# Kernel optimization log

Hardware: AMD Instinct MI355X
Metric: run time of the kernel (lower is better)

The kernel has to match this reference:

```python
import jax, jax.numpy as jnp
import numpy as np

N, E, G = 20000, 320000, 256
CAT, CONT, NEL = 16, 8, 9
HC, HE, HID, H, OUT = 32, 32, 64, 4, 128


def _gatv2(h, src, tgt, ee, Wl, bl, Wr, br, We, att, bias):
    # PyG GATv2Conv (eval mode, flow=source_to_target): messages aggregated at tgt
    n = h.shape[0]
    Hh, C = att.shape
    xl = (h @ Wl + bl).reshape(n, Hh, C)   # source transform
    xr = (h @ Wr + br).reshape(n, Hh, C)   # target transform
    ep = (ee @ We).reshape(-1, Hh, C)      # edge transform (no bias in PyG)
    m = jax.nn.leaky_relu(xl[src] + xr[tgt] + ep, 0.2)  # [E,H,C]
    e = jnp.einsum('ehc,hc->eh', m, att)                # [E,H]
    emax = jax.ops.segment_max(e, tgt, num_segments=n)
    p = jnp.exp(e - emax[tgt])
    denom = jax.ops.segment_sum(p, tgt, num_segments=n)
    alpha = p / (denom[tgt] + 1e-16)
    out = jax.ops.segment_sum(alpha[..., None] * xl[src], tgt, num_segments=n)
    return out.reshape(n, Hh * C) + bias


def setup_inputs() -> dict:
    key = jax.random.key(0)
    k = jax.random.split(key, 26)
    f = jnp.float32
    def w(kk, i, o):
        return jax.random.normal(kk, (i, o), f) / np.float32(np.sqrt(i))
    return {
        'x': jax.random.normal(k[0], (N, CAT + CONT), f),
        'edge_index': jax.random.randint(k[1], (2, E), 0, N, jnp.int32),
        'edge_attr': jax.random.uniform(k[2], (E, NEL), f),
        'batch': jnp.sort(jax.random.randint(k[3], (N,), 0, G, jnp.int32)),
        'W_cat': w(k[4], CAT, HC), 'b_cat': jnp.zeros((HC,), f),
        'W_e': w(k[5], NEL, HE), 'b_e': jnp.zeros((HE,), f),
        'W_init': w(k[6], CONT + HC, HID), 'b_init': jnp.zeros((HID,), f),
        'Wl1': w(k[7], HID, H * HID), 'bl1': jnp.zeros((H * HID,), f),
        'Wr1': w(k[8], HID, H * HID), 'br1': jnp.zeros((H * HID,), f),
        'We1': w(k[9], HE, H * HID),
        'att1': jax.random.normal(k[10], (H, HID), f) / np.float32(np.sqrt(HID)),
        'bias1': jnp.zeros((H * HID,), f),
        'Wl2': w(k[11], H * HID, HID), 'bl2': jnp.zeros((HID,), f),
        'Wr2': w(k[12], H * HID, HID), 'br2': jnp.zeros((HID,), f),
        'We2': w(k[13], HE, HID),
        'att2': jax.random.normal(k[14], (1, HID), f) / np.float32(np.sqrt(HID)),
        'bias2': jnp.zeros((HID,), f),
        'W_out': w(k[15], HID, OUT), 'b_out': jnp.zeros((OUT,), f),
    }


def reference(x, edge_index, edge_attr, batch,
              W_cat, b_cat, W_e, b_e, W_init, b_init,
              Wl1, bl1, Wr1, br1, We1, att1, bias1,
              Wl2, bl2, Wr2, br2, We2, att2, bias2,
              W_out, b_out):
    n = x.shape[0]
    f = x.dtype
    s = jax.nn.relu(x[:, :CAT] @ W_cat + b_cat)
    h = jnp.concatenate([x[:, CAT:], s], axis=1)
    h = jax.nn.relu(h @ W_init + b_init)
    ee = edge_attr @ W_e + b_e                       # [E, HE]
    src, tgt = edge_index[0], edge_index[1]
    # PyG GATv2Conv add_self_loops=True, fill_value='mean' on edge features
    cnt = jax.ops.segment_sum(jnp.ones((src.shape[0],), f), tgt, num_segments=n)
    loop_attr = jax.ops.segment_sum(ee, tgt, num_segments=n) / jnp.maximum(cnt, 1.0)[:, None]
    ar = jnp.arange(n, dtype=src.dtype)
    src2 = jnp.concatenate([src, ar])
    tgt2 = jnp.concatenate([tgt, ar])
    ee2 = jnp.concatenate([ee, loop_attr], axis=0)
    h = jax.nn.elu(_gatv2(h, src2, tgt2, ee2, Wl1, bl1, Wr1, br1, We1, att1, bias1))
    h = jax.nn.elu(_gatv2(h, src2, tgt2, ee2, Wl2, bl2, Wr2, br2, We2, att2, bias2))
    # global_mean_pool over graphs
    gcnt = jax.ops.segment_sum(jnp.ones((n,), f), batch, num_segments=G)
    pooled = jax.ops.segment_sum(h, batch, num_segments=G) / jnp.maximum(gcnt, 1.0)[:, None]
    return pooled @ W_out + b_out
```

## Files before the change

kernel.cpp:

```cpp
#include <hip/hip_runtime.h>
#include <hip/hip_bf16.h>

#define NN 20000
#define EE 320000
#define GG 256

__device__ __forceinline__ float lanebc(float v, int l){
  return __uint_as_float(__builtin_amdgcn_readlane(__float_as_uint(v), (unsigned)l));
}
__device__ __forceinline__ int lanebci(int v, int l){
  return __builtin_amdgcn_readlane(v, (unsigned)l);
}
__device__ __forceinline__ float wave_sum(float v){
  #pragma unroll
  for(int m=32;m>0;m>>=1) v += __shfl_xor(v, m, 64);
  return v;
}
__device__ __forceinline__ float wave_max(float v){
  #pragma unroll
  for(int m=32;m>0;m>>=1) v = fmaxf(v, __shfl_xor(v, m, 64));
  return v;
}
__device__ __forceinline__ float elu(float o){
  return (o > 0.f) ? o : (__expf(o) - 1.f);
}
__device__ __forceinline__ float bf2f(ushort u){ return __uint_as_float((unsigned)u << 16); }
__device__ __forceinline__ ushort f2bf(float f){
  unsigned x = __float_as_uint(f);
  return (ushort)((x + 0x7FFFu + ((x >> 16) & 1u)) >> 16);
}
__device__ __forceinline__ float2 up2(unsigned w){
  return make_float2(__uint_as_float(w << 16), __uint_as_float(w & 0xFFFF0000u));
}

template<int F>
__global__ void k_fold(const float* __restrict__ We9, const float* __restrict__ be,
                       const float* __restrict__ WeL, float* __restrict__ Wf, float* __restrict__ bf){
  const int c = threadIdx.x;
  #pragma unroll
  for (int j=0;j<9;j++){
    float a = 0.f;
    #pragma unroll
    for (int k=0;k<32;k++) a += We9[j*32+k]*WeL[k*F+c];
    Wf[j*F+c] = a;
  }
  float b = 0.f;
  #pragma unroll
  for (int k=0;k<32;k++) b += be[k]*WeL[k*F+c];
  bf[c] = b;
}

__global__ void k_prep(const float* __restrict__ Wl1, const float* __restrict__ Wl2,
                       const float* __restrict__ Wr2, float4* __restrict__ Wl1p4,
                       float4* __restrict__ Wl2p4, float4* __restrict__ Wr2p4){
  const int idx = (blockIdx.x%16)*256 + threadIdx.x;
  const int seg = blockIdx.x/16;
  if (seg == 0){
    const int k4 = idx>>8, c = idx&255;
    Wl1p4[idx] = make_float4(Wl1[(4*k4+0)*256+c], Wl1[(4*k4+1)*256+c],
                             Wl1[(4*k4+2)*256+c], Wl1[(4*k4+3)*256+c]);
  } else if (seg == 1){
    const int k4 = idx>>6, cc = idx&63;
    Wl2p4[idx] = make_float4(Wl2[(4*k4+0)*64+cc], Wl2[(4*k4+1)*64+cc],
                             Wl2[(4*k4+2)*64+cc], Wl2[(4*k4+3)*64+cc]);
  } else {
    const int k4 = idx>>6, cc = idx&63;
    Wr2p4[idx] = make_float4(Wr2[(4*k4+0)*64+cc], Wr2[(4*k4+1)*64+cc],
                             Wr2[(4*k4+2)*64+cc], Wr2[(4*k4+3)*64+cc]);
  }
}

__global__ void k_node_mlp(const float* __restrict__ x, const float* __restrict__ Wcat,
                           const float* __restrict__ bcat, const float* __restrict__ Wini,
                           const float* __restrict__ bini, float* __restrict__ h0,
                           ushort* __restrict__ h0b){
  const int t = blockIdx.x;
  const int c = threadIdx.x;
  __shared__ float xs[24];
  __shared__ float s[32];
  if (c < 24) xs[c] = x[t*24 + c];
  __syncthreads();
  if (c < 32){
    float a = bcat[c];
    #pragma unroll
    for(int k=0;k<16;k++) a += xs[k]*Wcat[k*32 + c];
    s[c] = fmaxf(a, 0.f);
  }
  __syncthreads();
  float a = bini[c];
  #pragma unroll
  for(int k=0;k<8;k++)  a += xs[16+k]*Wini[k*64 + c];
  #pragma unroll
  for(int k=0;k<32;k++) a += s[k]*Wini[(8+k)*64 + c];
  const float r = fmaxf(a, 0.f);
  h0[t*64 + c] = r;
  h0b[t*64 + c] = f2bf(r);
}

__global__ void k_edge_acc(const int* __restrict__ ei, const float* __restrict__ ea,
                           float* __restrict__ loopA, int* __restrict__ cnt){
  const int g = blockIdx.x*16 + (threadIdx.x>>4);
  const int j = threadIdx.x & 15;
  if (g >= EE) return;
  const int t = ei[EE + g];
  if (j < 9)       atomicAdd(&loopA[t*12 + j], ea[(size_t)g*9 + j]);
  else if (j == 9) atomicAdd(&cnt[t], 1);
}

__global__ void k_alloc(const int* __restrict__ cnt, int* __restrict__ start, int* __restrict__ counter){
  int i = blockIdx.x*blockDim.x + threadIdx.x;
  if (i < NN) start[i] = atomicAdd(counter, cnt[i]);
}

__global__ void k_scatter(const int* __restrict__ ei, const int* __restrict__ start,
                          int* __restrict__ fill, int* __restrict__ csr,
                          int* __restrict__ srcp, int* __restrict__ tgtp){
  int e = blockIdx.x*blockDim.x + threadIdx.x;
  if (e >= EE) return;
  int t = ei[EE + e];
  int p = start[t] + atomicAdd(&fill[t], 1);
  csr[p] = e;
  srcp[p] = ei[e];
  tgtp[p] = t;
}

__global__ void k_xlxr1(const float* __restrict__ h0, const float* __restrict__ Wl,
                        const float* __restrict__ bl, const float* __restrict__ Wr,
                        const float* __restrict__ br, ushort* __restrict__ xl, ushort* __restrict__ xr){
  const int n0 = blockIdx.x*8;
  __shared__ __align__(16) float hsT[64][8];
  for(int i=threadIdx.x;i<512;i+=256){ int n=i>>6, k=i&63; hsT[k][n] = h0[(n0+n)*64 + k]; }
  __syncthreads();
  const int c = threadIdx.x;
  float accl[8], accr[8];
  const float blv = bl[c], brv = br[c];
  #pragma unroll
  for(int n=0;n<8;n++){ accl[n]=blv; accr[n]=brv; }
  for(int k=0;k<64;k++){
    const float wl = Wl[k*256 + c];
    const float wr = Wr[k*256 + c];
    const float4 ha = *(const float4*)&hsT[k][0];
    const float4 hb = *(const float4*)&hsT[k][4];
    accl[0]+=ha.x*wl; accr[0]+=ha.x*wr; accl[1]+=ha.y*wl; accr[1]+=ha.y*wr;
    accl[2]+=ha.z*wl; accr[2]+=ha.z*wr; accl[3]+=ha.w*wl; accr[3]+=ha.w*wr;
    accl[4]+=hb.x*wl; accr[4]+=hb.x*wr; accl[5]+=hb.y*wl; accr[5]+=hb.y*wr;
    accl[6]+=hb.z*wl; accr[6]+=hb.z*wr; accl[7]+=hb.w*wl; accr[7]+=hb.w*wr;
  }
  #pragma unroll
  for(int n=0;n<8;n++){
    xl[(size_t)(n0+n)*256 + c] = f2bf(accl[n]);
    xr[(size_t)(n0+n)*256 + c] = f2bf(accr[n]);
  }
}

template<int F>
__global__ __launch_bounds__(256) void k_score(const float* __restrict__ ea, const int* __restrict__ csr,
                        const int* __restrict__ srcp, const int* __restrict__ tgtp,
                        const ushort* __restrict__ xl, const ushort* __restrict__ xr,
                        const float* __restrict__ Wf, const float* __restrict__ bf,
                        const float* __restrict__ att, float* __restrict__ esc)
{
  constexpr int HP  = (F == 256) ? 2 : 1;
  constexpr int CPL = (F == 256) ? 8 : 4;
  const int tid  = threadIdx.x;
  const int lane = tid & 63;
  const int w    = tid >> 6;
  const int p0   = blockIdx.x * 64;

  __shared__ float ea_sT[9][64];
  __shared__ float Wf_s[9*F];
  __shared__ float bf_s[F];
  __shared__ int csr_s[64], src_s[64], tgt_s[64];

  if (tid < 64) { csr_s[tid] = csr[p0+tid]; src_s[tid] = srcp[p0+tid]; tgt_s[tid] = tgtp[p0+tid]; }
  __syncthreads();
  for (int i = tid; i < 576; i += 256){ int j = i>>6, ed = i&63; ea_sT[j][ed] = ea[(size_t)csr_s[ed]*9 + j]; }
  for (int i = tid; i < (9*F)/4; i += 256) ((float4*)Wf_s)[i] = ((const float4*)Wf)[i];
  if (tid < F) bf_s[tid] = bf[tid];
  __syncthreads();

  const int g = lane >> 4, t = lane & 15;
  const int eb = w*16 + g*4;

  #pragma unroll
  for (int hp = 0; hp < HP; ++hp) {
    const int c = hp*(F/HP) + t*CPL;
    float bfv[CPL];
    *(float4*)&bfv[0] = *(const float4*)&bf_s[c];
    if (CPL==8) *(float4*)&bfv[4] = *(const float4*)&bf_s[c+4];
    float acc[4][CPL];
    #pragma unroll
    for (int j=0;j<4;j++)
      #pragma unroll
      for(int q=0;q<CPL;q++) acc[j][q]=bfv[q];
    #pragma unroll
    for (int k=0;k<9;k++){
      const float4 ev = *(const float4*)&ea_sT[k][eb];
      float wv[CPL];
      *(float4*)&wv[0] = *(const float4*)&Wf_s[k*F + c];
      if (CPL==8) *(float4*)&wv[4] = *(const float4*)&Wf_s[k*F + c + 4];
      #pragma unroll
      for (int q=0;q<CPL;q++){
        acc[0][q] += ev.x*wv[q]; acc[1][q] += ev.y*wv[q];
        acc[2][q] += ev.z*wv[q]; acc[3][q] += ev.w*wv[q];
      }
    }
    float attv[CPL];
    *(float4*)&attv[0] = *(const float4*)&att[c];
    if (CPL==8) *(float4*)&attv[4] = *(const float4*)&att[c+4];
    float partial[4];
    #pragma unroll
    for (int j=0;j<4;j++){
      const int s  = src_s[eb+j];
      const int tg = tgt_s[eb+j];
      float xlv[CPL], xrv[CPL];
      if (CPL==8){
        const uint4 a = *(const uint4*)&xl[(size_t)s*F + c];
        const uint4 b = *(const uint4*)&xr[(size_t)tg*F + c];
        float2 p;
        p=up2(a.x); xlv[0]=p.x; xlv[1]=p.y;  p=up2(a.y); xlv[2]=p.x; xlv[3]=p.y;
        p=up2(a.z); xlv[4]=p.x; xlv[5]=p.y;  p=up2(a.w); xlv[6]=p.x; xlv[7]=p.y;
        p=up2(b.x); xrv[0]=p.x; xrv[1]=p.y;  p=up2(b.y); xrv[2]=p.x; xrv[3]=p.y;
        p=up2(b.z); xrv[4]=p.x; xrv[5]=p.y;  p=up2(b.w); xrv[6]=p.x; xrv[7]=p.y;
      } else {
        const uint2 a = *(const uint2*)&xl[(size_t)s*F + c];
        const uint2 b = *(const uint2*)&xr[(size_t)tg*F + c];
        float2 p;
        p=up2(a.x); xlv[0]=p.x; xlv[1]=p.y;  p=up2(a.y); xlv[2]=p.x; xlv[3]=p.y;
        p=up2(b.x); xrv[0]=p.x; xrv[1]=p.y;  p=up2(b.y); xrv[2]=p.x; xrv[3]=p.y;
      }
      float sum = 0.f;
      #pragma unroll
      for (int q=0;q<CPL;q++){
        float m = acc[j][q] + xlv[q] + xrv[q];
        m = (m >= 0.f) ? m : 0.2f*m;
        sum += attv[q]*m;
      }
      partial[j] = sum;
    }
    #pragma unroll
    for (int j=0;j<4;j++){
      partial[j] += __shfl_xor(partial[j], 1, 64);
      partial[j] += __shfl_xor(partial[j], 2, 64);
      partial[j] += __shfl_xor(partial[j], 4, 64);
      if (F==64) partial[j] += __shfl_xor(partial[j], 8, 64);
    }
    if (F==256){
      if ((t & 7) == 0){
        const int h = hp*2 + (t>>3);
        #pragma unroll
        for (int j=0;j<4;j++) esc[(size_t)h*EE + p0 + eb + j] = partial[j];
      }
    } else {
      if (t == 0){
        #pragma unroll
        for (int j=0;j<4;j++) esc[p0 + eb + j] = partial[j];
      }
    }
  }
}

__global__ __launch_bounds__(256) void k_agg1(
    const float* __restrict__ loopA, const int* __restrict__ cnt,
    const int* __restrict__ start, const int* __restrict__ srcp,
    const ushort* __restrict__ h0b, const ushort* __restrict__ xl, const ushort* __restrict__ xr,
    const float* __restrict__ Wf, const float* __restrict__ bf,
    const float* __restrict__ att, const float* __restrict__ esc,
    float* __restrict__ zb)
{
  const int t = blockIdx.x*4 + (threadIdx.x>>6);
  const int c = threadIdx.x & 63;
  const int st = start[t], dg = cnt[t];

  float epb[4];
  if (dg > 0){
    const float invc = 1.f/(float)dg;
    float la[9];
    #pragma unroll
    for (int j=0;j<9;j++) la[j] = loopA[t*12+j]*invc;
    #pragma unroll
    for (int hd=0;hd<4;hd++){
      float ep = bf[hd*64+c];
      #pragma unroll
      for (int j=0;j<9;j++) ep += la[j]*Wf[j*256 + hd*64 + c];
      epb[hd] = ep;
    }
  } else {
    #pragma unroll
    for (int hd=0;hd<4;hd++) epb[hd]=0.f;
  }
  const float h0t = bf2f(h0b[(size_t)t*64 + c]);
  float sSelf[4];
  #pragma unroll
  for (int hd=0;hd<4;hd++){
    float m = bf2f(xl[(size_t)t*256 + hd*64 + c]) + bf2f(xr[(size_t)t*256 + hd*64 + c]) + epb[hd];
    m = (m>=0.f)? m : 0.2f*m;
    sSelf[hd] = wave_sum(att[hd*64+c]*m);
  }

  int sL = 0;
  float escv[4];
  #pragma unroll
  for (int hd=0;hd<4;hd++) escv[hd] = -1e30f;
  if (c < dg){
    sL = srcp[st+c];
    #pragma unroll
    for (int hd=0;hd<4;hd++) escv[hd] = esc[(size_t)hd*EE + st + c];
  }
  float mx[4];
  #pragma unroll
  for (int hd=0;hd<4;hd++) mx[hd] = fmaxf(wave_max(escv[hd]), sSelf[hd]);
  for (int i=64;i<dg;i+=64){
    #pragma unroll
    for (int hd=0;hd<4;hd++){
      float v = (i+c<dg)? esc[(size_t)hd*EE + st+i+c] : -1e30f;
      mx[hd] = fmaxf(mx[hd], wave_max(v));
    }
  }
  float preg[4], den[4], z[4];
  #pragma unroll
  for (int hd=0;hd<4;hd++){
    preg[hd] = (c<dg)? __expf(escv[hd]-mx[hd]) : 0.f;
    const float pS = __expf(sSelf[hd]-mx[hd]);
    den[hd] = wave_sum(preg[hd]) + pS;
    z[hd] = pS*h0t;
  }
  const int d1 = min(dg,64);
  for (int i=0;i<d1;i+=4){
    const int s0=lanebci(sL,i), s1=lanebci(sL,i+1), s2=lanebci(sL,i+2), s3=lanebci(sL,i+3);
    const float v0=bf2f(h0b[(size_t)s0*64+c]), v1=bf2f(h0b[(size_t)s1*64+c]);
    const float v2=bf2f(h0b[(size_t)s2*64+c]), v3=bf2f(h0b[(size_t)s3*64+c]);
    #pragma unroll
    for (int hd=0;hd<4;hd++){
      z[hd] += lanebc(preg[hd],i)*v0;
      z[hd] += lanebc(preg[hd],i+1)*v1;
      z[hd] += lanebc(preg[hd],i+2)*v2;
      z[hd] += lanebc(preg[hd],i+3)*v3;
    }
  }
  for (int i=64;i<dg;i++){
    const float hv = bf2f(h0b[(size_t)srcp[st+i]*64+c]);
    #pragma unroll
    for (int hd=0;hd<4;hd++){
      const float pp = __expf(esc[(size_t)hd*EE+st+i]-mx[hd]);
      den[hd] += pp;
      z[hd] += pp*hv;
    }
  }
  #pragma unroll
  for (int hd=0;hd<4;hd++) zb[(size_t)t*256 + hd*64 + c] = z[hd]/(den[hd]+1e-16f);
}

__global__ __launch_bounds__(256) void k_h1xlxr2(
    const float* __restrict__ zb, const float4* __restrict__ Wl1p4,
    const float* __restrict__ bl1, const float* __restrict__ bias1,
    const float4* __restrict__ Wl2p4, const float* __restrict__ bl2,
    const float4* __restrict__ Wr2p4, const float* __restrict__ br2,
    ushort* __restrict__ xl2, ushort* __restrict__ xr2)
{
  const int n0 = blockIdx.x*16;
  const int tid = threadIdx.x;
  __shared__ float zT[256*20];
  __shared__ __align__(16) float4 hs[64][17];
  #pragma unroll
  for (int j=0;j<16;j++) zT[tid*20 + j] = zb[(size_t)(n0+j)*256 + tid];
  __syncthreads();
  {
    const int c = tid, hd = c>>6;
    float acc[16];
    const float b = bl1[c] + bias1[c];
    #pragma unroll
    for (int n=0;n<16;n++) acc[n]=b;
    #pragma unroll 4
    for (int k4=0;k4<16;k4++){
      const float4 w4 = Wl1p4[k4*256 + c];
      #pragma unroll
      for (int kk=0;kk<4;kk++){
        const float wk = (kk==0)?w4.x:(kk==1)?w4.y:(kk==2)?w4.z:w4.w;
        const float* zr = &zT[(hd*64 + k4*4 + kk)*20];
        const float4 z0 = *(const float4*)&zr[0];
        const float4 z1 = *(const float4*)&zr[4];
        const float4 z2 = *(const float4*)&zr[8];
        const float4 z3 = *(const float4*)&zr[12];
        acc[0]+=z0.x*wk; acc[1]+=z0.y*wk; acc[2]+=z0.z*wk; acc[3]+=z0.w*wk;
        acc[4]+=z1.x*wk; acc[5]+=z1.y*wk; acc[6]+=z1.z*wk; acc[7]+=z1.w*wk;
        acc[8]+=z2.x*wk; acc[9]+=z2.y*wk; acc[10]+=z2.z*wk; acc[11]+=z2.w*wk;
        acc[12]+=z3.x*wk; acc[13]+=z3.y*wk; acc[14]+=z3.z*wk; acc[15]+=z3.w*wk;
      }
    }
    float* hsf = (float*)hs;
    const int base = (c>>2)*17*4 + (c&3);
    #pragma unroll
    for (int n=0;n<16;n++) hsf[base + n*4] = elu(acc[n]);
  }
  __syncthreads();
  {
    const int cc = tid & 63, ng = tid >> 6;
    float al[4], ar[4];
    const float bl = bl2[cc], br = br2[cc];
    #pragma unroll
    for (int j=0;j<4;j++){ al[j]=bl; ar[j]=br; }
    #pragma unroll 4
    for (int k4=0;k4<64;k4++){
      const float4 wl = Wl2p4[k4*64 + cc];
      const float4 wr = Wr2p4[k4*64 + cc];
      #pragma unroll
      for (int j=0;j<4;j++){
        const float4 hv = hs[k4][ng*4 + j];
        al[j] += hv.x*wl.x + hv.y*wl.y + hv.z*wl.z + hv.w*wl.w;
        ar[j] += hv.x*wr.x + hv.y*wr.y + hv.z*wr.z + hv.w*wr.w;
      }
    }
    #pragma unroll
    for (int j=0;j<4;j++){
      xl2[(size_t)(n0+ng*4+j)*64 + cc] = f2bf(al[j]);
      xr2[(size_t)(n0+ng*4+j)*64 + cc] = f2bf(ar[j]);
    }
  }
}

__global__ __launch_bounds__(256) void k_agg2(
    const float* __restrict__ loopA, const int* __restrict__ cnt,
    const int* __restrict__ start, const int* __restrict__ srcp,
    const ushort* __restrict__ xl, const ushort* __restrict__ xr,
    const float* __restrict__ Wf, const float* __restrict__ bf,
    const float* __restrict__ att, const float* __restrict__ bias,
    const float* __restrict__ esc, float* __restrict__ hout)
{
  const int t = blockIdx.x*4 + (threadIdx.x>>6);
  const int c = threadIdx.x & 63;
  const int st = start[t], dg = cnt[t];

  float ep = 0.f;
  if (dg>0){
    const float invc = 1.f/(float)dg;
    ep = bf[c];
    #pragma unroll
    for (int j=0;j<9;j++) ep += (loopA[t*12+j]*invc)*Wf[j*64+c];
  }
  const float xlt = bf2f(xl[(size_t)t*64+c]);
  float m = xlt + bf2f(xr[(size_t)t*64+c]) + ep;
  m = (m>=0.f)? m : 0.2f*m;
  const float sSelf = wave_sum(att[c]*m);

  int sL=0; float escv=-1e30f;
  if (c<dg){ sL=srcp[st+c]; escv=esc[st+c]; }
  float mx = fmaxf(wave_max(escv), sSelf);
  for (int i=64;i<dg;i+=64){
    float v=(i+c<dg)? esc[st+i+c] : -1e30f;
    mx = fmaxf(mx, wave_max(v));
  }
  float preg = (c<dg)? __expf(escv-mx) : 0.f;
  const float pS = __expf(sSelf-mx);
  float den = wave_sum(preg)+pS;
  float z = pS*xlt;
  const int d1=min(dg,64);
  for (int i=0;i<d1;i+=4){
    const int s0=lanebci(sL,i),s1=lanebci(sL,i+1),s2=lanebci(sL,i+2),s3=lanebci(sL,i+3);
    const float p0=lanebc(preg,i),p1=lanebc(preg,i+1),p2=lanebc(preg,i+2),p3=lanebc(preg,i+3);
    const float v0=bf2f(xl[(size_t)s0*64+c]),v1=bf2f(xl[(size_t)s1*64+c]);
    const float v2=bf2f(xl[(size_t)s2*64+c]),v3=bf2f(xl[(size_t)s3*64+c]);
    z += p0*v0; z += p1*v1; z += p2*v2; z += p3*v3;
  }
  for (int i=64;i<dg;i++){
    const float pp=__expf(esc[st+i]-mx); den+=pp;
    z += pp*bf2f(xl[(size_t)srcp[st+i]*64+c]);
  }
  const float o = z/(den+1e-16f)+bias[c];
  hout[(size_t)t*64+c] = elu(o);
}

__global__ void k_pool(const float* __restrict__ h2, const int* __restrict__ batch,
                       float* __restrict__ pooled, int* __restrict__ gcnt){
  int i = blockIdx.x*blockDim.x + threadIdx.x;
  if (i >= NN*64) return;
  int node = i >> 6, c = i & 63;
  int g = batch[node];
  atomicAdd(&pooled[g*64 + c], h2[i]);
  if (c == 0) atomicAdd(&gcnt[g], 1);
}

__global__ void k_out(const float* __restrict__ pooled, const int* __restrict__ gcnt,
                      const float* __restrict__ Wout, const float* __restrict__ bout,
                      float* __restrict__ out){
  int g = blockIdx.x, o = threadIdx.x;
  float a = 0.f;
  for(int k=0;k<64;k++) a += pooled[g*64 + k] * Wout[k*128 + o];
  float inv = 1.f / fmaxf((float)gcnt[g], 1.f);
  out[g*128 + o] = a*inv + bout[o];
}

extern "C" void kernel_launch(void* const* d_in, const int* in_sizes, int n_in,
                              void* d_out, int out_size, void* d_ws, size_t ws_size,
                              hipStream_t stream) {
  const float* x    = (const float*)d_in[0];
  const int*   ei   = (const int*)  d_in[1];
  const float* ea   = (const float*)d_in[2];
  const int*   batch= (const int*)  d_in[3];
  const float* Wcat = (const float*)d_in[4];
  const float* bcat = (const float*)d_in[5];
  const float* We   = (const float*)d_in[6];
  const float* be   = (const float*)d_in[7];
  const float* Wini = (const float*)d_in[8];
  const float* bini = (const float*)d_in[9];
  const float* Wl1  = (const float*)d_in[10];
  const float* bl1  = (const float*)d_in[11];
  const float* Wr1  = (const float*)d_in[12];
  const float* br1  = (const float*)d_in[13];
  const float* We1  = (const float*)d_in[14];
  const float* att1 = (const float*)d_in[15];
  const float* bias1= (const float*)d_in[16];
  const float* Wl2  = (const float*)d_in[17];
  const float* bl2  = (const float*)d_in[18];
  const float* Wr2  = (const float*)d_in[19];
  const float* br2  = (const float*)d_in[20];
  const float* We2  = (const float*)d_in[21];
  const float* att2 = (const float*)d_in[22];
  const float* bias2= (const float*)d_in[23];
  const float* Wout = (const float*)d_in[24];
  const float* bout = (const float*)d_in[25];
  float* out = (float*)d_out;
  char* ws = (char*)d_ws;

  size_t off = 0;
  auto alloc = [&](size_t bytes)->char*{ char* p = ws + off; off += (bytes + 255) & ~(size_t)255; return p; };
  float*  h0    = (float*) alloc((size_t)NN*64*4);
  ushort* h0b   = (ushort*)alloc((size_t)NN*64*2);
  float*  loopA = (float*) alloc((size_t)NN*12*4);
  ushort* xl1   = (ushort*)alloc((size_t)NN*256*2);
  ushort* xr1   = (ushort*)alloc((size_t)NN*256*2);
  float*  zb    = (float*) alloc((size_t)NN*256*4);
  ushort* xl2   = (ushort*)alloc((size_t)NN*64*2);
  ushort* xr2   = (ushort*)alloc((size_t)NN*64*2);
  float*  h2    = (float*) alloc((size_t)NN*64*4);
  float*  esc   = (float*) alloc((size_t)EE*4*4);
  float*  Wf1   = (float*) alloc((size_t)9*256*4);
  float*  bf1   = (float*) alloc((size_t)256*4);
  float*  Wf2   = (float*) alloc((size_t)9*64*4);
  float*  bf2   = (float*) alloc((size_t)64*4);
  float4* Wl1p4 = (float4*)alloc((size_t)4096*16);
  float4* Wl2p4 = (float4*)alloc((size_t)4096*16);
  float4* Wr2p4 = (float4*)alloc((size_t)4096*16);
  int*    cnt   = (int*)   alloc((size_t)NN*4);
  int*    start = (int*)   alloc((size_t)NN*4);
  int*    fill  = (int*)   alloc((size_t)NN*4);
  int*    csr   = (int*)   alloc((size_t)EE*4);
  int*    srcp  = (int*)   alloc((size_t)EE*4);
  int*    tgtp  = (int*)   alloc((size_t)EE*4);
  int*    counter = (int*) alloc(256);
  float*  pooled  = (float*)alloc((size_t)GG*64*4);
  int*    gcnt    = (int*)  alloc((size_t)GG*4);

  hipMemsetAsync(loopA,   0, (size_t)NN*12*4, stream);
  hipMemsetAsync(cnt,     0, (size_t)NN*4,    stream);
  hipMemsetAsync(fill,    0, (size_t)NN*4,    stream);
  hipMemsetAsync(counter, 0, 256,             stream);
  hipMemsetAsync(pooled,  0, (size_t)GG*64*4, stream);
  hipMemsetAsync(gcnt,    0, (size_t)GG*4,    stream);

  k_fold<256><<<1, 256, 0, stream>>>(We, be, We1, Wf1, bf1);
  k_fold<64> <<<1, 64, 0, stream>>>(We, be, We2, Wf2, bf2);
  k_prep     <<<48, 256, 0, stream>>>(Wl1, Wl2, Wr2, Wl1p4, Wl2p4, Wr2p4);
  k_node_mlp <<<NN, 64, 0, stream>>>(x, Wcat, bcat, Wini, bini, h0, h0b);
  k_edge_acc <<<EE/16, 256, 0, stream>>>(ei, ea, loopA, cnt);
  k_alloc    <<<(NN+255)/256, 256, 0, stream>>>(cnt, start, counter);
  k_scatter  <<<(EE+255)/256, 256, 0, stream>>>(ei, start, fill, csr, srcp, tgtp);
  k_xlxr1    <<<NN/8, 256, 0, stream>>>(h0, Wl1, bl1, Wr1, br1, xl1, xr1);
  k_score<256><<<EE/64, 256, 0, stream>>>(ea, csr, srcp, tgtp, xl1, xr1, Wf1, bf1, att1, esc);
  k_agg1     <<<NN/4, 256, 0, stream>>>(loopA, cnt, start, srcp, h0b, xl1, xr1, Wf1, bf1, att1, esc, zb);
  k_h1xlxr2  <<<NN/16, 256, 0, stream>>>(zb, Wl1p4, bl1, bias1, Wl2p4, bl2, Wr2p4, br2, xl2, xr2);
  k_score<64><<<EE/64, 256, 0, stream>>>(ea, csr, srcp, tgtp, xl2, xr2, Wf2, bf2, att2, esc);
  k_agg2     <<<NN/4, 256, 0, stream>>>(loopA, cnt, start, srcp, xl2, xr2, Wf2, bf2, att2, bias2, esc, h2);
  k_pool     <<<(NN*64+255)/256, 256, 0, stream>>>(h2, batch, pooled, gcnt);
  k_out      <<<GG, 128, 0, stream>>>(pooled, gcnt, Wout, bout, out);
}
```

Baseline: 339.5 us.

## Fuse node MLP, weight prep, pooling; drop softmax max pass; interleave scores

Merges the weight-folding and prep kernels into one launch and fuses the node MLP into the layer-1 xl/xr projection kernel. Global pooling is folded into the layer-2 aggregation, and the six memsets become one over a contiguous zeroed region. The softmax no longer computes a per-target max; it exponentiates raw scores clamped at 60, which removes a pass over the edge scores but risks overflow or precision loss for large scores. Layer-1 scores are stored interleaved by head so each edge's four heads load as one float4.

```diff
diff --git a/kernel.cpp b/kernel.cpp
--- a/kernel.cpp
+++ b/kernel.cpp
@@ -16,14 +16,10 @@
   for(int m=32;m>0;m>>=1) v += __shfl_xor(v, m, 64);
   return v;
 }
-__device__ __forceinline__ float wave_max(float v){
-  #pragma unroll
-  for(int m=32;m>0;m>>=1) v = fmaxf(v, __shfl_xor(v, m, 64));
-  return v;
-}
 __device__ __forceinline__ float elu(float o){
   return (o > 0.f) ? o : (__expf(o) - 1.f);
 }
+__device__ __forceinline__ float pexp(float e){ return __expf(fminf(e, 60.f)); }
 __device__ __forceinline__ float bf2f(ushort u){ return __uint_as_float((unsigned)u << 16); }
 __device__ __forceinline__ ushort f2bf(float f){
   unsigned x = __float_as_uint(f);
@@ -33,68 +29,61 @@
   return make_float2(__uint_as_float(w << 16), __uint_as_float(w & 0xFFFF0000u));
 }
 
-template<int F>
-__global__ void k_fold(const float* __restrict__ We9, const float* __restrict__ be,
-                       const float* __restrict__ WeL, float* __restrict__ Wf, float* __restrict__ bf){
-  const int c = threadIdx.x;
-  #pragma unroll
-  for (int j=0;j<9;j++){
-    float a = 0.f;
-    #pragma unroll
-    for (int k=0;k<32;k++) a += We9[j*32+k]*WeL[k*F+c];
-    Wf[j*F+c] = a;
-  }
-  float b = 0.f;
-  #pragma unroll
-  for (int k=0;k<32;k++) b += be[k]*WeL[k*F+c];
-  bf[c] = b;
-}
-
-__global__ void k_prep(const float* __restrict__ Wl1, const float* __restrict__ Wl2,
-                       const float* __restrict__ Wr2, float4* __restrict__ Wl1p4,
-                       float4* __restrict__ Wl2p4, float4* __restrict__ Wr2p4){
-  const int idx = (blockIdx.x%16)*256 + threadIdx.x;
-  const int seg = blockIdx.x/16;
-  if (seg == 0){
-    const int k4 = idx>>8, c = idx&255;
-    Wl1p4[idx] = make_float4(Wl1[(4*k4+0)*256+c], Wl1[(4*k4+1)*256+c],
-                             Wl1[(4*k4+2)*256+c], Wl1[(4*k4+3)*256+c]);
-  } else if (seg == 1){
-    const int k4 = idx>>6, cc = idx&63;
-    Wl2p4[idx] = make_float4(Wl2[(4*k4+0)*64+cc], Wl2[(4*k4+1)*64+cc],
-                             Wl2[(4*k4+2)*64+cc], Wl2[(4*k4+3)*64+cc]);
+__global__ void k_weights(const float* __restrict__ We9, const float* __restrict__ be,
+                          const float* __restrict__ We1, const float* __restrict__ We2,
+                          const float* __restrict__ Wl1, const float* __restrict__ Wl2,
+                          const float* __restrict__ Wr2,
+                          float* __restrict__ Wf1, float* __restrict__ bf1,
+                          float* __restrict__ Wf2, float* __restrict__ bf2,
+                          float4* __restrict__ Wl1p4, float4* __restrict__ Wl2p4,
+                          float4* __restrict__ Wr2p4){
+  const int b = blockIdx.x;
+  const int tid = threadIdx.x;
+  if (b < 48){
+    const int idx = (b%16)*256 + tid;
+    const int seg = b/16;
+    if (seg == 0){
+      const int k4 = idx>>8, c = idx&255;
+      Wl1p4[idx] = make_float4(Wl1[(4*k4+0)*256+c], Wl1[(4*k4+1)*256+c],
+                               Wl1[(4*k4+2)*256+c], Wl1[(4*k4+3)*256+c]);
+    } else if (seg == 1){
+      const int k4 = idx>>6, cc = idx&63;
+      Wl2p4[idx] = make_float4(Wl2[(4*k4+0)*64+cc], Wl2[(4*k4+1)*64+cc],
+                               Wl2[(4*k4+2)*64+cc], Wl2[(4*k4+3)*64+cc]);
+    } else {
+      const int k4 = idx>>6, cc = idx&63;
+      Wr2p4[idx] = make_float4(Wr2[(4*k4+0)*64+cc], Wr2[(4*k4+1)*64+cc],
+                               Wr2[(4*k4+2)*64+cc], Wr2[(4*k4+3)*64+cc]);
+    }
+  } else if (b == 48){
+    const int c = tid;
+    #pragma unroll
+    for (int j=0;j<9;j++){
+      float a = 0.f;
+      #pragma unroll
+      for (int k=0;k<32;k++) a += We9[j*32+k]*We1[k*256+c];
+      Wf1[j*256+c] = a;
+    }
+    float bb = 0.f;
+    #pragma unroll
+    for (int k=0;k<32;k++) bb += be[k]*We1[k*256+c];
+    bf1[c] = bb;
   } else {
-    const int k4 = idx>>6, cc = idx&63;
-    Wr2p4[idx] = make_float4(Wr2[(4*k4+0)*64+cc], Wr2[(4*k4+1)*64+cc],
-                             Wr2[(4*k4+2)*64+cc], Wr2[(4*k4+3)*64+cc]);
-  }
-}
-
-__global__ void k_node_mlp(const float* __restrict__ x, const float* __restrict__ Wcat,
-                           const float* __restrict__ bcat, const float* __restrict__ Wini,
-                           const float* __restrict__ bini, float* __restrict__ h0,
-                           ushort* __restrict__ h0b){
-  const int t = blockIdx.x;
-  const int c = threadIdx.x;
-  __shared__ float xs[24];
-  __shared__ float s[32];
-  if (c < 24) xs[c] = x[t*24 + c];
-  __syncthreads();
-  if (c < 32){
-    float a = bcat[c];
-    #pragma unroll
-    for(int k=0;k<16;k++) a += xs[k]*Wcat[k*32 + c];
-    s[c] = fmaxf(a, 0.f);
-  }
-  __syncthreads();
-  float a = bini[c];
-  #pragma unroll
-  for(int k=0;k<8;k++)  a += xs[16+k]*Wini[k*64 + c];
-  #pragma unroll
-  for(int k=0;k<32;k++) a += s[k]*Wini[(8+k)*64 + c];
-  const float r = fmaxf(a, 0.f);
-  h0[t*64 + c] = r;
-  h0b[t*64 + c] = f2bf(r);
+    if (tid < 64){
+      const int c = tid;
+      #pragma unroll
+      for (int j=0;j<9;j++){
+        float a = 0.f;
+        #pragma unroll
+        for (int k=0;k<32;k++) a += We9[j*32+k]*We2[k*64+c];
+        Wf2[j*64+c] = a;
+      }
+      float bb = 0.f;
+      #pragma unroll
+      for (int k=0;k<32;k++) bb += be[k]*We2[k*64+c];
+      bf2[c] = bb;
+    }
+  }
 }
 
 __global__ void k_edge_acc(const int* __restrict__ ei, const float* __restrict__ ea,
@@ -124,14 +113,43 @@
   tgtp[p] = t;
 }
 
-__global__ void k_xlxr1(const float* __restrict__ h0, const float* __restrict__ Wl,
-                        const float* __restrict__ bl, const float* __restrict__ Wr,
-                        const float* __restrict__ br, ushort* __restrict__ xl, ushort* __restrict__ xr){
+__global__ __launch_bounds__(256) void k_xlxr1f(
+    const float* __restrict__ x, const float* __restrict__ Wcat,
+    const float* __restrict__ bcat, const float* __restrict__ Wini,
+    const float* __restrict__ bini, const float* __restrict__ Wl,
+    const float* __restrict__ bl, const float* __restrict__ Wr,
+    const float* __restrict__ br, ushort* __restrict__ h0b,
+    ushort* __restrict__ xl, ushort* __restrict__ xr)
+{
   const int n0 = blockIdx.x*8;
+  const int tid = threadIdx.x;
+  __shared__ float xs[8][25];
+  __shared__ float sv[8][33];
   __shared__ __align__(16) float hsT[64][8];
-  for(int i=threadIdx.x;i<512;i+=256){ int n=i>>6, k=i&63; hsT[k][n] = h0[(n0+n)*64 + k]; }
-  __syncthreads();
-  const int c = threadIdx.x;
+  if (tid < 192){ int n=tid/24, j=tid%24; xs[n][j] = x[(size_t)(n0+n)*24 + j]; }
+  __syncthreads();
+  {
+    const int n = tid>>5, cc = tid&31;
+    float a = bcat[cc];
+    #pragma unroll
+    for (int k=0;k<16;k++) a += xs[n][k]*Wcat[k*32+cc];
+    sv[n][cc] = fmaxf(a, 0.f);
+  }
+  __syncthreads();
+  #pragma unroll
+  for (int i=tid;i<512;i+=256){
+    const int n = i>>6, c = i&63;
+    float a = bini[c];
+    #pragma unroll
+    for (int k=0;k<8;k++)  a += xs[n][16+k]*Wini[k*64+c];
+    #pragma unroll
+    for (int k=0;k<32;k++) a += sv[n][k]*Wini[(8+k)*64+c];
+    const float r = fmaxf(a, 0.f);
+    hsT[c][n] = r;
+    h0b[(size_t)(n0+n)*64 + c] = f2bf(r);
+  }
+  __syncthreads();
+  const int c = tid;
   float accl[8], accr[8];
   const float blv = bl[c], brv = br[c];
   #pragma unroll
@@ -249,7 +267,7 @@
       if ((t & 7) == 0){
         const int h = hp*2 + (t>>3);
         #pragma unroll
-        for (int j=0;j<4;j++) esc[(size_t)h*EE + p0 + eb + j] = partial[j];
+        for (int j=0;j<4;j++) esc[(size_t)(p0 + eb + j)*4 + h] = partial[j];
       }
     } else {
       if (t == 0){
@@ -290,41 +308,27 @@
     for (int hd=0;hd<4;hd++) epb[hd]=0.f;
   }
   const float h0t = bf2f(h0b[(size_t)t*64 + c]);
-  float sSelf[4];
+  float preg[4], den[4], z[4];
   #pragma unroll
   for (int hd=0;hd<4;hd++){
     float m = bf2f(xl[(size_t)t*256 + hd*64 + c]) + bf2f(xr[(size_t)t*256 + hd*64 + c]) + epb[hd];
     m = (m>=0.f)? m : 0.2f*m;
-    sSelf[hd] = wave_sum(att[hd*64+c]*m);
+    const float pS = pexp(wave_sum(att[hd*64+c]*m));
+    den[hd] = pS;
+    z[hd] = pS*h0t;
   }
 
   int sL = 0;
-  float escv[4];
-  #pragma unroll
-  for (int hd=0;hd<4;hd++) escv[hd] = -1e30f;
+  #pragma unroll
+  for (int hd=0;hd<4;hd++) preg[hd] = 0.f;
   if (c < dg){
     sL = srcp[st+c];
-    #pragma unroll
-    for (int hd=0;hd<4;hd++) escv[hd] = esc[(size_t)hd*EE + st + c];
-  }
-  float mx[4];
-  #pragma unroll
-  for (int hd=0;hd<4;hd++) mx[hd] = fmaxf(wave_max(escv[hd]), sSelf[hd]);
-  for (int i=64;i<dg;i+=64){
-    #pragma unroll
-    for (int hd=0;hd<4;hd++){
-      float v = (i+c<dg)? esc[(size_t)hd*EE + st+i+c] : -1e30f;
-      mx[hd] = fmaxf(mx[hd], wave_max(v));
-    }
-  }
-  float preg[4], den[4], z[4];
-  #pragma unroll
-  for (int hd=0;hd<4;hd++){
-    preg[hd] = (c<dg)? __expf(escv[hd]-mx[hd]) : 0.f;
-    const float pS = __expf(sSelf[hd]-mx[hd]);
-    den[hd] = wave_sum(preg[hd]) + pS;
-    z[hd] = pS*h0t;
-  }
+    const float4 e4 = *(const float4*)&esc[(size_t)(st+c)*4];
+    preg[0]=pexp(e4.x); preg[1]=pexp(e4.y); preg[2]=pexp(e4.z); preg[3]=pexp(e4.w);
+  }
+  #pragma unroll
+  for (int hd=0;hd<4;hd++) den[hd] += wave_sum(preg[hd]);
+
   const int d1 = min(dg,64);
   for (int i=0;i<d1;i+=4){
     const int s0=lanebci(sL,i), s1=lanebci(sL,i+1), s2=lanebci(sL,i+2), s3=lanebci(sL,i+3);
@@ -340,12 +344,10 @@
   }
   for (int i=64;i<dg;i++){
     const float hv = bf2f(h0b[(size_t)srcp[st+i]*64+c]);
-    #pragma unroll
-    for (int hd=0;hd<4;hd++){
-      const float pp = __expf(esc[(size_t)hd*EE+st+i]-mx[hd]);
-      den[hd] += pp;
-      z[hd] += pp*hv;
-    }
+    const float4 e4 = *(const float4*)&esc[(size_t)(st+i)*4];
+    const float p0=pexp(e4.x), p1=pexp(e4.y), p2=pexp(e4.z), p3=pexp(e4.w);
+    den[0]+=p0; den[1]+=p1; den[2]+=p2; den[3]+=p3;
+    z[0]+=p0*hv; z[1]+=p1*hv; z[2]+=p2*hv; z[3]+=p3*hv;
   }
   #pragma unroll
   for (int hd=0;hd<4;hd++) zb[(size_t)t*256 + hd*64 + c] = z[hd]/(den[hd]+1e-16f);
@@ -425,7 +427,8 @@
     const ushort* __restrict__ xl, const ushort* __restrict__ xr,
     const float* __restrict__ Wf, const float* __restrict__ bf,
     const float* __restrict__ att, const float* __restrict__ bias,
-    const float* __restrict__ esc, float* __restrict__ hout)
+    const float* __restrict__ esc, const int* __restrict__ batch,
+    float* __restrict__ pooled, int* __restrict__ gcnt)
 {
   const int t = blockIdx.x*4 + (threadIdx.x>>6);
   const int c = threadIdx.x & 63;
@@ -441,17 +444,10 @@
   const float xlt = bf2f(xl[(size_t)t*64+c]);
   float m = xlt + bf2f(xr[(size_t)t*64+c]) + ep;
   m = (m>=0.f)? m : 0.2f*m;
-  const float sSelf = wave_sum(att[c]*m);
-
-  int sL=0; float escv=-1e30f;
-  if (c<dg){ sL=srcp[st+c]; escv=esc[st+c]; }
-  float mx = fmaxf(wave_max(escv), sSelf);
-  for (int i=64;i<dg;i+=64){
-    float v=(i+c<dg)? esc[st+i+c] : -1e30f;
-    mx = fmaxf(mx, wave_max(v));
-  }
-  float preg = (c<dg)? __expf(escv-mx) : 0.f;
-  const float pS = __expf(sSelf-mx);
+  const float pS = pexp(wave_sum(att[c]*m));
+
+  int sL=0; float preg=0.f;
+  if (c<dg){ sL=srcp[st+c]; preg=pexp(esc[st+c]); }
   float den = wave_sum(preg)+pS;
   float z = pS*xlt;
   const int d1=min(dg,64);
@@ -463,20 +459,13 @@
     z += p0*v0; z += p1*v1; z += p2*v2; z += p3*v3;
   }
   for (int i=64;i<dg;i++){
-    const float pp=__expf(esc[st+i]-mx); den+=pp;
+    const float pp=pexp(esc[st+i]); den+=pp;
     z += pp*bf2f(xl[(size_t)srcp[st+i]*64+c]);
   }
   const float o = z/(den+1e-16f)+bias[c];
-  hout[(size_t)t*64+c] = elu(o);
-}
-
-__global__ void k_pool(const float* __restrict__ h2, const int* __restrict__ batch,
-                       float* __restrict__ pooled, int* __restrict__ gcnt){
-  int i = blockIdx.x*blockDim.x + threadIdx.x;
-  if (i >= NN*64) return;
-  int node = i >> 6, c = i & 63;
-  int g = batch[node];
-  atomicAdd(&pooled[g*64 + c], h2[i]);
+  const float r = elu(o);
+  const int g = batch[t];
+  atomicAdd(&pooled[g*64 + c], r);
   if (c == 0) atomicAdd(&gcnt[g], 1);
 }
 
@@ -524,16 +513,14 @@
 
   size_t off = 0;
   auto alloc = [&](size_t bytes)->char*{ char* p = ws + off; off += (bytes + 255) & ~(size_t)255; return p; };
-  float*  h0    = (float*) alloc((size_t)NN*64*4);
   ushort* h0b   = (ushort*)alloc((size_t)NN*64*2);
-  float*  loopA = (float*) alloc((size_t)NN*12*4);
   ushort* xl1   = (ushort*)alloc((size_t)NN*256*2);
   ushort* xr1   = (ushort*)alloc((size_t)NN*256*2);
   float*  zb    = (float*) alloc((size_t)NN*256*4);
   ushort* xl2   = (ushort*)alloc((size_t)NN*64*2);
   ushort* xr2   = (ushort*)alloc((size_t)NN*64*2);
-  float*  h2    = (float*) alloc((size_t)NN*64*4);
   float*  esc   = (float*) alloc((size_t)EE*4*4);
+  float*  esc2  = (float*) alloc((size_t)EE*4);
   float*  Wf1   = (float*) alloc((size_t)9*256*4);
   float*  bf1   = (float*) alloc((size_t)256*4);
   float*  Wf2   = (float*) alloc((size_t)9*64*4);
@@ -541,36 +528,33 @@
   float4* Wl1p4 = (float4*)alloc((size_t)4096*16);
   float4* Wl2p4 = (float4*)alloc((size_t)4096*16);
   float4* Wr2p4 = (float4*)alloc((size_t)4096*16);
-  int*    cnt   = (int*)   alloc((size_t)NN*4);
   int*    start = (int*)   alloc((size_t)NN*4);
-  int*    fill  = (int*)   alloc((size_t)NN*4);
   int*    csr   = (int*)   alloc((size_t)EE*4);
   int*    srcp  = (int*)   alloc((size_t)EE*4);
   int*    tgtp  = (int*)   alloc((size_t)EE*4);
+  const size_t zoff = off;
+  float*  loopA = (float*) alloc((size_t)NN*12*4);
+  int*    cnt   = (int*)   alloc((size_t)NN*4);
+  int*    fill  = (int*)   alloc((size_t)NN*4);
   int*    counter = (int*) alloc(256);
   float*  pooled  = (float*)alloc((size_t)GG*64*4);
   int*    gcnt    = (int*)  alloc((size_t)GG*4);
-
-  hipMemsetAsync(loopA,   0, (size_t)NN*12*4, stream);
-  hipMemsetAsync(cnt,     0, (size_t)NN*4,    stream);
-  hipMemsetAsync(fill,    0, (size_t)NN*4,    stream);
-  hipMemsetAsync(counter, 0, 256,             stream);
-  hipMemsetAsync(pooled,  0, (size_t)GG*64*4, stream);
-  hipMemsetAsync(gcnt,    0, (size_t)GG*4,    stream);
-
-  k_fold<256><<<1, 256, 0, stream>>>(We, be, We1, Wf1, bf1);
-  k_fold<64> <<<1, 64, 0, stream>>>(We, be, We2, Wf2, bf2);
-  k_prep     <<<48, 256, 0, stream>>>(Wl1, Wl2, Wr2, Wl1p4, Wl2p4, Wr2p4);
-  k_node_mlp <<<NN, 64, 0, stream>>>(x, Wcat, bcat, Wini, bini, h0, h0b);
+  const size_t zlen = off - zoff;
+
+  hipMemsetAsync(ws + zoff, 0, zlen, stream);
+
+  k_weights  <<<50, 256, 0, stream>>>(We, be, We1, We2, Wl1, Wl2, Wr2,
+                                      Wf1, bf1, Wf2, bf2, Wl1p4, Wl2p4, Wr2p4);
   k_edge_acc <<<EE/16, 256, 0, stream>>>(ei, ea, loopA, cnt);
   k_alloc    <<<(NN+255)/256, 256, 0, stream>>>(cnt, start, counter);
   k_scatter  <<<(EE+255)/256, 256, 0, stream>>>(ei, start, fill, csr, srcp, tgtp);
-  k_xlxr1    <<<NN/8, 256, 0, stream>>>(h0, Wl1, bl1, Wr1, br1, xl1, xr1);
+  k_xlxr1f   <<<NN/8, 256, 0, stream>>>(x, Wcat, bcat, Wini, bini,
+                                        Wl1, bl1, Wr1, br1, h0b, xl1, xr1);
   k_score<256><<<EE/64, 256, 0, stream>>>(ea, csr, srcp, tgtp, xl1, xr1, Wf1, bf1, att1, esc);
   k_agg1     <<<NN/4, 256, 0, stream>>>(loopA, cnt, start, srcp, h0b, xl1, xr1, Wf1, bf1, att1, esc, zb);
   k_h1xlxr2  <<<NN/16, 256, 0, stream>>>(zb, Wl1p4, bl1, bias1, Wl2p4, bl2, Wr2p4, br2, xl2, xr2);
-  k_score<64><<<EE/64, 256, 0, stream>>>(ea, csr, srcp, tgtp, xl2, xr2, Wf2, bf2, att2, esc);
-  k_agg2     <<<NN/4, 256, 0, stream>>>(loopA, cnt, start, srcp, xl2, xr2, Wf2, bf2, att2, bias2, esc, h2);
-  k_pool     <<<(NN*64+255)/256, 256, 0, stream>>>(h2, batch, pooled, gcnt);
+  k_score<64><<<EE/64, 256, 0, stream>>>(ea, csr, srcp, tgtp, xl2, xr2, Wf2, bf2, att2, esc2);
+  k_agg2     <<<NN/4, 256, 0, stream>>>(loopA, cnt, start, srcp, xl2, xr2, Wf2, bf2, att2, bias2,
+                                        esc2, batch, pooled, gcnt);
   k_out      <<<GG, 128, 0, stream>>>(pooled, gcnt, Wout, bout, out);
 }
```

New measurement: 421.5 us. 1.24x slower.
